# Optimization experiments

Measured on AMD Instinct MI355X. Metric: run time of the kernel, lower is better.

The kernel has to match this reference:

```python
import jax, jax.numpy as jnp
import numpy as np

N = 60000   # nodes
E = 200000  # edges
D = 128     # hidden_dim
H = 4       # heads
C = 128     # out_channels per head (concat=False)
L = 3       # num_layers
VA = 128    # atom vocab
VB = 16     # bond vocab
NEG_SLOPE = 0.2


def setup_inputs():
    key = jax.random.key(0)
    ks = jax.random.split(key, 12)
    f = lambda k, s: (jax.random.normal(k, s, jnp.float32) * 0.05)
    return dict(
        x=jax.random.randint(ks[0], (N,), 0, VA),
        edge_index=jax.random.randint(ks[1], (2, E), 0, N),
        edge_attr=jax.random.randint(ks[2], (E,), 0, VB),
        atom_emb=f(ks[3], (VA, D)),
        bond_emb=f(ks[4], (VB, D)),
        Wl=f(ks[5], (L, D, H * C)), bl=jnp.zeros((L, H * C), jnp.float32),
        Wr=f(ks[6], (L, D, H * C)), br=jnp.zeros((L, H * C), jnp.float32),
        We=f(ks[7], (L, D, H * C)),
        att=f(ks[8], (L, H, C)),
        bias=jnp.zeros((L, C), jnp.float32),
        Wa=f(ks[9], (D, VA)), ba=jnp.zeros((VA,), jnp.float32),
        Wb=f(ks[10], (2 * D, VB)), bb=jnp.zeros((VB,), jnp.float32),
    )


def _gatv2_layer(h, e, src, dst, Wl, bl, Wr, br, We, att, bias):
    # GATv2Conv (PyG), eval mode (dropout off), concat=False -> mean over heads
    xl = (h @ Wl + bl).reshape(N, H, C)   # source transform (lin_l)
    xr = (h @ Wr + br).reshape(N, H, C)   # target transform (lin_r)
    ee = (e @ We).reshape(E, H, C)        # edge projection (lin_edge, no bias)
    m = jax.nn.leaky_relu(xl[src] + xr[dst] + ee, NEG_SLOPE)  # [E,H,C]
    logits = jnp.einsum('ehc,hc->eh', m, att)                 # [E,H]
    # segment-softmax over incoming edges of each target node
    mx = jax.ops.segment_max(logits, dst, num_segments=N)
    a = jnp.exp(logits - mx[dst])
    s = jax.ops.segment_sum(a, dst, num_segments=N)
    alpha = a / (s[dst] + 1e-16)
    agg = jax.ops.segment_sum(alpha[:, :, None] * xl[src], dst, num_segments=N)
    return agg.mean(axis=1) + bias  # [N,D]


def reference(x, edge_index, edge_attr, atom_emb, bond_emb,
              Wl, bl, Wr, br, We, att, bias, Wa, ba, Wb, bb):
    src, dst = edge_index[0], edge_index[1]
    h = atom_emb[x]          # [N,D]
    e = bond_emb[edge_attr]  # [E,D]
    for l in range(L):
        upd = _gatv2_layer(h, e, src, dst, Wl[l], bl[l], Wr[l], br[l],
                           We[l], att[l], bias[l])
        h = h + jax.nn.relu(upd)
    atom_logits = h @ Wa + ba                              # [N,VA]
    pair = jnp.concatenate([h[src], h[dst]], axis=-1)      # [E,2D]
    bond_logits = pair @ Wb + bb                           # [E,VB]
    return atom_logits, bond_logits
```

## Files before the change

kernel.cpp:

```cpp
#include <hip/hip_runtime.h>
#include <hip/hip_bf16.h>
#include <math.h>

#define NN 60000
#define NE 200000
#define DD 128
#define NH 4
#define HC 512
#define NL 3
#define VAv 128
#define VBv 16
#define SCAN_CHUNK 512

typedef __attribute__((ext_vector_type(8))) short bf16x8;
typedef __attribute__((ext_vector_type(4))) float f32x4;

__device__ __forceinline__ float bf2f(unsigned short u){
    union{unsigned int i; float f;} v; v.i = ((unsigned int)u)<<16; return v.f;
}
__device__ __forceinline__ unsigned short f2bf(float f){
    union{float f; unsigned int i;} v; v.f = f;
    unsigned int r = v.i + 0x7fffu + ((v.i>>16)&1u);
    return (unsigned short)(r>>16);
}

#define GLOAD_LDS16(g, l) \
    __builtin_amdgcn_global_load_lds((const __attribute__((address_space(1))) void*)(g), \
                                     (__attribute__((address_space(3))) void*)(l), 16, 0, 0)

__global__ void k_embed(const int* __restrict__ x, const float* __restrict__ atom_emb,
                        float* __restrict__ h, unsigned short* __restrict__ hb) {
    int idx = blockIdx.x*blockDim.x + threadIdx.x;
    if (idx >= NN*(DD/4)) return;
    int n = idx >> 5;
    int c4 = idx & 31;
    int a = x[n];
    float4 v = ((const float4*)(atom_emb + (size_t)a*DD))[c4];
    ((float4*)(h + (size_t)n*DD))[c4] = v;
    ushort4 u = make_ushort4(f2bf(v.x), f2bf(v.y), f2bf(v.z), f2bf(v.w));
    ((ushort4*)(hb + (size_t)n*DD))[c4] = u;
}

__global__ void k_convw(const float* __restrict__ Wl, const float* __restrict__ Wr,
                        const float* __restrict__ bl, const float* __restrict__ br,
                        unsigned short* __restrict__ Wlrt, float* __restrict__ blr) {
    int t = blockIdx.x*256 + threadIdx.x;
    if (t < NL*1024*DD) {
        int l = t / (1024*DD);
        int r = t % (1024*DD);
        int n = r / DD;
        int k = r % DD;
        float v = (n < HC) ? Wl[(size_t)l*DD*HC + (size_t)k*HC + n]
                           : Wr[(size_t)l*DD*HC + (size_t)k*HC + (n - HC)];
        Wlrt[t] = f2bf(v);
    }
    if (t < NL*1024) {
        int l = t / 1024, j = t % 1024;
        blr[t] = (j < HC) ? bl[(size_t)l*HC + j] : br[(size_t)l*HC + (j - HC)];
    }
}

__global__ void k_convwa(const float* __restrict__ Wa, unsigned short* __restrict__ Wat) {
    int t = blockIdx.x*256 + threadIdx.x;
    if (t >= DD*VAv) return;
    int n = t / DD;
    int k = t % DD;
    Wat[t] = f2bf(Wa[(size_t)k*VAv + n]);
}

__global__ void k_eproj(const float* __restrict__ bond_emb, const float* __restrict__ We,
                        float* __restrict__ eprojd) {
    int t = blockIdx.x*256 + threadIdx.x;
    if (t >= NL*VBv*HC) return;
    int n = t & (HC-1);
    int v = (t >> 9) & (VBv-1);
    int l = t >> 13;
    const float* be = bond_emb + (size_t)v*DD;
    const float* w  = We + (size_t)l*DD*HC + n;
    float acc = 0.f;
    #pragma unroll 8
    for (int k = 0; k < DD; ++k) acc = fmaf(be[k], w[(size_t)k*HC], acc);
    int ln = n >> 3, u = n & 7;
    int pos = (u >> 2)*256 + ln*4 + (u & 3);
    eprojd[((size_t)l*VBv + v)*HC + pos] = acc;
}

__global__ void k_deg(const int* __restrict__ dst, int* __restrict__ deg) {
    int e = blockIdx.x*blockDim.x + threadIdx.x;
    if (e < NE) atomicAdd(&deg[dst[e]], 1);
}

__global__ void k_scan1(const int* __restrict__ deg, int* __restrict__ exc, int* __restrict__ sums) {
    __shared__ int buf[2][SCAN_CHUNK];
    int t = threadIdx.x;
    int gi = blockIdx.x*SCAN_CHUNK + t;
    int v = (gi < NN) ? deg[gi] : 0;
    buf[0][t] = v;
    __syncthreads();
    int cur = 0;
    for (int off = 1; off < SCAN_CHUNK; off <<= 1) {
        int nv = buf[cur][t] + ((t >= off) ? buf[cur][t-off] : 0);
        buf[cur^1][t] = nv;
        __syncthreads();
        cur ^= 1;
    }
    if (gi < NN) exc[gi] = buf[cur][t] - v;
    if (t == SCAN_CHUNK-1) sums[blockIdx.x] = buf[cur][t];
}

__global__ void k_scan2(int* sums, int nb) {
    __shared__ int buf[2][128];
    int t = threadIdx.x;
    int v = (t < nb) ? sums[t] : 0;
    buf[0][t] = v;
    __syncthreads();
    int cur = 0;
    for (int off = 1; off < 128; off <<= 1) {
        int nv = buf[cur][t] + ((t >= off) ? buf[cur][t-off] : 0);
        buf[cur^1][t] = nv;
        __syncthreads();
        cur ^= 1;
    }
    if (t < nb) sums[t] = buf[cur][t] - v;
}

__global__ void k_scan3(const int* __restrict__ exc, const int* __restrict__ sums,
                        int* __restrict__ rowptr) {
    int i = blockIdx.x*blockDim.x + threadIdx.x;
    if (i < NN) rowptr[i] = exc[i] + sums[i / SCAN_CHUNK];
    if (i == NN) rowptr[NN] = NE;
}

__global__ void k_scatter(const int* __restrict__ srcv, const int* __restrict__ dst,
                          const int* __restrict__ eattr, const int* __restrict__ rowptr,
                          int* __restrict__ cnt, int* __restrict__ packed) {
    int e = blockIdx.x*blockDim.x + threadIdx.x;
    if (e < NE) {
        int d = dst[e];
        int pos = atomicAdd(&cnt[d], 1);
        packed[rowptr[d] + pos] = srcv[e] | (eattr[e] << 16);
    }
}

template<bool OUT_BF16, int MT>
__global__ __launch_bounds__(256)
void k_gemm_mfma(const unsigned short* __restrict__ A,
                 const unsigned short* __restrict__ Bt,
                 const float* __restrict__ bias, void* __restrict__ Cout,
                 int M, int Nc) {
    __shared__ unsigned short As[2][128*128];
    const int tid = threadIdx.x;
    const int lane = tid & 63;
    const int wave = tid >> 6;
    const int bn = blockIdx.x * 128;
    const int bm0 = blockIdx.y * (128*MT);
    const int l15 = lane & 15;
    const int l4  = lane >> 4;
    const int wm = (wave >> 1) * 64;
    const int wn = (wave & 1) * 64;

    bf16x8 bfr[4][4];
    #pragma unroll
    for (int ks = 0; ks < 4; ++ks)
        #pragma unroll
        for (int ni = 0; ni < 4; ++ni)
            bfr[ks][ni] = *(const bf16x8*)(Bt + (size_t)(bn + wn + ni*16 + l15)*128
                                              + (size_t)(ks*4 + l4)*8);

    float4 bv[4];
    #pragma unroll
    for (int ni = 0; ni < 4; ++ni)
        bv[ni] = bias ? *(const float4*)(bias + bn + wn + ni*16 + l4*4)
                      : make_float4(0.f, 0.f, 0.f, 0.f);

    auto stage = [&](int buf, int bm) {
        #pragma unroll
        for (int it = 0; it < 8; ++it) {
            int slot = it*256 + tid;
            int row  = slot >> 4;
            int cph  = slot & 15;
            int clog = cph ^ (row & 15);
            int arow = bm + row; if (arow >= M) arow = M - 1;
            unsigned short* ldst = &As[buf][(size_t)(it*256 + (tid & ~63))*8];
            GLOAD_LDS16(A + (size_t)arow*128 + clog*8, ldst);
        }
    };

    stage(0, bm0);
    asm volatile("s_waitcnt vmcnt(0)" ::: "memory");
    __syncthreads();

    int cur = 0;
    for (int t = 0; t < MT; ++t) {
        int bm = bm0 + t*128;
        if (bm >= M) break;
        bool pf = (t+1 < MT) && (bm + 128 < M);
        if (pf) stage(cur^1, bm + 128);

        f32x4 acc[4][4];
        #pragma unroll
        for (int i = 0; i < 4; ++i)
            #pragma unroll
            for (int j = 0; j < 4; ++j)
                acc[i][j] = (f32x4){0.f, 0.f, 0.f, 0.f};

        #pragma unroll
        for (int ks = 0; ks < 4; ++ks) {
            bf16x8 af[4];
            int cph = (ks*4 + l4) ^ l15;
            #pragma unroll
            for (int mi = 0; mi < 4; ++mi) {
                int row = wm + mi*16 + l15;
                af[mi] = *(const bf16x8*)(&As[cur][(size_t)row*128 + cph*8]);
            }
            #pragma unroll
            for (int mi = 0; mi < 4; ++mi)
                #pragma unroll
                for (int ni = 0; ni < 4; ++ni)
                    acc[mi][ni] = __builtin_amdgcn_mfma_f32_16x16x32_bf16(bfr[ks][ni], af[mi], acc[mi][ni], 0, 0, 0);
        }

        #pragma unroll
        for (int mi = 0; mi < 4; ++mi) {
            int row = bm + wm + mi*16 + l15;
            bool rok = (row < M);
            #pragma unroll
            for (int ni = 0; ni < 4; ++ni) {
                float v0 = acc[mi][ni][0] + bv[ni].x;
                float v1 = acc[mi][ni][1] + bv[ni].y;
                float v2 = acc[mi][ni][2] + bv[ni].z;
                float v3 = acc[mi][ni][3] + bv[ni].w;
                int colb = bn + wn + ni*16 + l4*4;
                if (rok) {
                    if (OUT_BF16) {
                        unsigned int lo, hi;
                        asm("v_cvt_pk_bf16_f32 %0, %1, %2" : "=v"(lo) : "v"(v0), "v"(v1));
                        asm("v_cvt_pk_bf16_f32 %0, %1, %2" : "=v"(hi) : "v"(v2), "v"(v3));
                        *(uint2*)((unsigned short*)Cout + (size_t)row*Nc + colb) = make_uint2(lo, hi);
                    } else {
                        *(float4*)((float*)Cout + (size_t)row*Nc + colb) = make_float4(v0, v1, v2, v3);
                    }
                }
            }
        }

        if (pf) {
            asm volatile("s_waitcnt vmcnt(16)" ::: "memory");
            __builtin_amdgcn_s_barrier();
        }
        cur ^= 1;
    }
}

__global__ __launch_bounds__(512)
void k_aggregate(const unsigned short* __restrict__ xlr,
                 const float* __restrict__ eprojd,
                 const int* __restrict__ rowptr, const int* __restrict__ packed,
                 const float* __restrict__ att,
                 const float* __restrict__ bias,
                 float* __restrict__ h, unsigned short* __restrict__ hb) {
    __shared__ float eps[VBv*HC];
    {
        const float4* s4 = (const float4*)eprojd;
        float4* d4 = (float4*)eps;
        int t = threadIdx.x;
        #pragma unroll
        for (int i = 0; i < 4; ++i) d4[t + i*512] = s4[t + i*512];
    }
    __syncthreads();

    const int wave = threadIdx.x >> 6;
    const int lane = threadIdx.x & 63;
    const int loff = lane*8;
    const int l4x  = lane*4;

    float attf[8];
    {
        float4 a0 = *(const float4*)(att + loff);
        float4 a1 = *(const float4*)(att + loff + 4);
        attf[0]=a0.x; attf[1]=a0.y; attf[2]=a0.z; attf[3]=a0.w;
        attf[4]=a1.x; attf[5]=a1.y; attf[6]=a1.z; attf[7]=a1.w;
    }

#define EDGE_PROC(vv, eA, eB) do {                                          \
        float xf_[8];                                                       \
        float epv_[8] = {eA.x,eA.y,eA.z,eA.w,eB.x,eB.y,eB.z,eB.w};          \
        float pz_ = 0.f;                                                    \
        _Pragma("unroll")                                                   \
        for (int u = 0; u < 8; ++u) {                                       \
            xf_[u] = bf2f((unsigned short)vv[u]);                           \
            float z_ = xf_[u] + xrf[u] + epv_[u];                           \
            pz_ = fmaf(fmaxf(z_, 0.2f*z_), attf[u], pz_);                   \
        }                                                                   \
        pz_ += __shfl_xor(pz_, 1);                                          \
        pz_ += __shfl_xor(pz_, 2);                                          \
        pz_ += __shfl_xor(pz_, 4);                                          \
        pz_ += __shfl_xor(pz_, 8);                                          \
        float w_ = __expf(pz_);                                             \
        wsum += w_;                                                         \
        _Pragma("unroll")                                                   \
        for (int u = 0; u < 8; ++u) acc[u] = fmaf(w_, xf_[u], acc[u]);      \
    } while (0)

    for (int g = blockIdx.x; g < NN/8; g += gridDim.x) {
        int n = g*8 + wave;

        float xrf[8];
        {
            bf16x8 xv = *(const bf16x8*)(xlr + (size_t)n*1024 + 512 + loff);
            #pragma unroll
            for (int u = 0; u < 8; ++u) xrf[u] = bf2f((unsigned short)xv[u]);
        }

        float acc[8] = {0,0,0,0,0,0,0,0};
        float wsum = 0.f;
        int beg = rowptr[n], end = rowptr[n+1];
        int p = beg;

        for (; p + 4 <= end; p += 4) {
            int pk0 = packed[p],   pk1 = packed[p+1];
            int pk2 = packed[p+2], pk3 = packed[p+3];
            bf16x8 v0 = *(const bf16x8*)(xlr + (size_t)(pk0 & 0xFFFF)*1024 + loff);
            bf16x8 v1 = *(const bf16x8*)(xlr + (size_t)(pk1 & 0xFFFF)*1024 + loff);
            bf16x8 v2 = *(const bf16x8*)(xlr + (size_t)(pk2 & 0xFFFF)*1024 + loff);
            bf16x8 v3 = *(const bf16x8*)(xlr + (size_t)(pk3 & 0xFFFF)*1024 + loff);
            const float* e0 = eps + (pk0 >> 16)*HC;
            const float* e1 = eps + (pk1 >> 16)*HC;
            const float* e2 = eps + (pk2 >> 16)*HC;
            const float* e3 = eps + (pk3 >> 16)*HC;
            float4 eA0 = *(const float4*)(e0 + l4x), eB0 = *(const float4*)(e0 + 256 + l4x);
            float4 eA1 = *(const float4*)(e1 + l4x), eB1 = *(const float4*)(e1 + 256 + l4x);
            float4 eA2 = *(const float4*)(e2 + l4x), eB2 = *(const float4*)(e2 + 256 + l4x);
            float4 eA3 = *(const float4*)(e3 + l4x), eB3 = *(const float4*)(e3 + 256 + l4x);
            EDGE_PROC(v0, eA0, eB0);
            EDGE_PROC(v1, eA1, eB1);
            EDGE_PROC(v2, eA2, eB2);
            EDGE_PROC(v3, eA3, eB3);
        }
        if (p + 2 <= end) {
            int pk0 = packed[p], pk1 = packed[p+1];
            bf16x8 v0 = *(const bf16x8*)(xlr + (size_t)(pk0 & 0xFFFF)*1024 + loff);
            bf16x8 v1 = *(const bf16x8*)(xlr + (size_t)(pk1 & 0xFFFF)*1024 + loff);
            const float* e0 = eps + (pk0 >> 16)*HC;
            const float* e1 = eps + (pk1 >> 16)*HC;
            float4 eA0 = *(const float4*)(e0 + l4x), eB0 = *(const float4*)(e0 + 256 + l4x);
            float4 eA1 = *(const float4*)(e1 + l4x), eB1 = *(const float4*)(e1 + 256 + l4x);
            EDGE_PROC(v0, eA0, eB0);
            EDGE_PROC(v1, eA1, eB1);
            p += 2;
        }
        if (p < end) {
            int pk0 = packed[p];
            bf16x8 v0 = *(const bf16x8*)(xlr + (size_t)(pk0 & 0xFFFF)*1024 + loff);
            const float* e0 = eps + (pk0 >> 16)*HC;
            float4 eA0 = *(const float4*)(e0 + l4x), eB0 = *(const float4*)(e0 + 256 + l4x);
            EDGE_PROC(v0, eA0, eB0);
        }

        float inv = __builtin_amdgcn_rcpf(wsum + 1e-16f);
        float rr[8];
        #pragma unroll
        for (int u = 0; u < 8; ++u) rr[u] = acc[u] * inv;
        #pragma unroll
        for (int u = 0; u < 8; ++u) rr[u] += __shfl_xor(rr[u], 16);
        #pragma unroll
        for (int u = 0; u < 8; ++u) rr[u] += __shfl_xor(rr[u], 32);

        if (lane < 16) {
            int c = lane*8;
            float* hp = h + (size_t)n*DD + c;
            float4 h0 = *(const float4*)hp;
            float4 h1 = *(const float4*)(hp + 4);
            float4 b0 = *(const float4*)(bias + c);
            float4 b1 = *(const float4*)(bias + c + 4);
            float o[8];
            o[0] = h0.x + fmaxf(0.f, fmaf(0.25f, rr[0], b0.x));
            o[1] = h0.y + fmaxf(0.f, fmaf(0.25f, rr[1], b0.y));
            o[2] = h0.z + fmaxf(0.f, fmaf(0.25f, rr[2], b0.z));
            o[3] = h0.w + fmaxf(0.f, fmaf(0.25f, rr[3], b0.w));
            o[4] = h1.x + fmaxf(0.f, fmaf(0.25f, rr[4], b1.x));
            o[5] = h1.y + fmaxf(0.f, fmaf(0.25f, rr[5], b1.y));
            o[6] = h1.z + fmaxf(0.f, fmaf(0.25f, rr[6], b1.z));
            o[7] = h1.w + fmaxf(0.f, fmaf(0.25f, rr[7], b1.w));
            *(float4*)hp       = make_float4(o[0], o[1], o[2], o[3]);
            *(float4*)(hp + 4) = make_float4(o[4], o[5], o[6], o[7]);
            ushort4 u0 = make_ushort4(f2bf(o[0]), f2bf(o[1]), f2bf(o[2]), f2bf(o[3]));
            ushort4 u1 = make_ushort4(f2bf(o[4]), f2bf(o[5]), f2bf(o[6]), f2bf(o[7]));
            unsigned short* hbp = hb + (size_t)n*DD + c;
            *(ushort4*)hbp       = u0;
            *(ushort4*)(hbp + 4) = u1;
        }
    }
#undef EDGE_PROC
}

__global__ __launch_bounds__(256)
void k_bond(const unsigned short* __restrict__ hb,
            const int* __restrict__ srcv, const int* __restrict__ dstv,
            const float* __restrict__ Wb, const float* __restrict__ bb,
            float* __restrict__ out) {
    int e = blockIdx.x*256 + threadIdx.x;
    if (e >= NE) return;
    int s = srcv[e], d = dstv[e];
    const bf16x8* hs = (const bf16x8*)(hb + (size_t)s*DD);
    const bf16x8* hd = (const bf16x8*)(hb + (size_t)d*DD);
    float acc[16];
    #pragma unroll
    for (int j = 0; j < 16; ++j) acc[j] = bb[j];
    for (int c = 0; c < 16; ++c) {
        bf16x8 v = hs[c];
        #pragma unroll
        for (int u = 0; u < 8; ++u) {
            float a = bf2f((unsigned short)v[u]);
            const float* w = Wb + (size_t)(c*8 + u)*16;
            #pragma unroll
            for (int j = 0; j < 16; ++j) acc[j] = fmaf(a, w[j], acc[j]);
        }
    }
    for (int c = 0; c < 16; ++c) {
        bf16x8 v = hd[c];
        #pragma unroll
        for (int u = 0; u < 8; ++u) {
            float a = bf2f((unsigned short)v[u]);
            const float* w = Wb + (size_t)(128 + c*8 + u)*16;
            #pragma unroll
            for (int j = 0; j < 16; ++j) acc[j] = fmaf(a, w[j], acc[j]);
        }
    }
    float4* o = (float4*)(out + (size_t)e*16);
    o[0] = make_float4(acc[0],  acc[1],  acc[2],  acc[3]);
    o[1] = make_float4(acc[4],  acc[5],  acc[6],  acc[7]);
    o[2] = make_float4(acc[8],  acc[9],  acc[10], acc[11]);
    o[3] = make_float4(acc[12], acc[13], acc[14], acc[15]);
}

extern "C" void kernel_launch(void* const* d_in, const int* in_sizes, int n_in,
                              void* d_out, int out_size, void* d_ws, size_t ws_size,
                              hipStream_t stream) {
    const int*   x        = (const int*)d_in[0];
    const int*   edge_idx = (const int*)d_in[1];
    const int*   eattr    = (const int*)d_in[2];
    const float* atom_emb = (const float*)d_in[3];
    const float* bond_emb = (const float*)d_in[4];
    const float* Wl  = (const float*)d_in[5];
    const float* bl  = (const float*)d_in[6];
    const float* Wr  = (const float*)d_in[7];
    const float* br  = (const float*)d_in[8];
    const float* We  = (const float*)d_in[9];
    const float* att = (const float*)d_in[10];
    const float* bias= (const float*)d_in[11];
    const float* Wa  = (const float*)d_in[12];
    const float* ba  = (const float*)d_in[13];
    const float* Wb  = (const float*)d_in[14];
    const float* bb  = (const float*)d_in[15];

    const int* src = edge_idx;
    const int* dst = edge_idx + NE;

    char* p = (char*)d_ws;
    auto alloc = [&](size_t bytes) -> void* {
        void* r = p; p += (bytes + 255) & ~(size_t)255; return r;
    };
    float*          h      = (float*)alloc((size_t)NN*DD*4);
    unsigned short* hb     = (unsigned short*)alloc((size_t)NN*DD*2);
    unsigned short* xlr    = (unsigned short*)alloc((size_t)NN*1024*2);
    unsigned short* Wlrt   = (unsigned short*)alloc((size_t)NL*1024*DD*2);
    float*          blr    = (float*)alloc((size_t)NL*1024*4);
    unsigned short* Wat    = (unsigned short*)alloc((size_t)DD*VAv*2);
    float*          eprojd = (float*)alloc((size_t)NL*VBv*HC*4);
    int*            deg    = (int*)alloc((size_t)NN*4);
    int*            exc    = (int*)alloc((size_t)NN*4);
    int*            sums   = (int*)alloc(256*4);
    int*            rowptr = (int*)alloc((size_t)(NN+1)*4);
    int*            cnt    = (int*)alloc((size_t)NN*4);
    int*            packed = (int*)alloc((size_t)NE*4);

    float* atom_out = (float*)d_out;
    float* bond_out = atom_out + (size_t)NN*VAv;

    hipMemsetAsync(deg, 0, (size_t)NN*4, stream);
    hipMemsetAsync(cnt, 0, (size_t)NN*4, stream);

    k_embed<<<7500, 256, 0, stream>>>(x, atom_emb, h, hb);
    k_convw<<<(NL*1024*DD + 255)/256, 256, 0, stream>>>(Wl, Wr, bl, br, Wlrt, blr);
    k_convwa<<<(DD*VAv + 255)/256, 256, 0, stream>>>(Wa, Wat);
    k_eproj<<<(NL*VBv*HC + 255)/256, 256, 0, stream>>>(bond_emb, We, eprojd);

    int nchunks = (NN + SCAN_CHUNK - 1) / SCAN_CHUNK;
    k_deg<<<(NE+255)/256, 256, 0, stream>>>(dst, deg);
    k_scan1<<<nchunks, SCAN_CHUNK, 0, stream>>>(deg, exc, sums);
    k_scan2<<<1, 128, 0, stream>>>(sums, nchunks);
    k_scan3<<<(NN+256)/256, 256, 0, stream>>>(exc, sums, rowptr);
    k_scatter<<<(NE+255)/256, 256, 0, stream>>>(src, dst, eattr, rowptr, cnt, packed);

    const int MTILES = (NN + 127) / 128;
    const int GRP4 = (MTILES + 3) / 4;
    const int GRP2 = (MTILES + 1) / 2;
    for (int l = 0; l < NL; ++l) {
        const float* att_l  = att  + (size_t)l*NH*VAv;
        const float* bias_l = bias + (size_t)l*DD;
        const unsigned short* Wlrt_l = Wlrt + (size_t)l*1024*DD;
        const float* blr_l = blr + (size_t)l*1024;
        const float* ep_l  = eprojd + (size_t)l*VBv*HC;

        k_gemm_mfma<true, 4><<<dim3(1024/128, GRP4), 256, 0, stream>>>(hb, Wlrt_l, blr_l, xlr, NN, 1024);
        k_aggregate<<<2500, 512, 0, stream>>>(xlr, ep_l, rowptr, packed, att_l, bias_l, h, hb);
    }

    k_gemm_mfma<false, 2><<<dim3(VAv/128, GRP2), 256, 0, stream>>>(hb, Wat, ba, atom_out, NN, VAv);
    k_bond<<<(NE+255)/256, 256, 0, stream>>>(hb, src, dst, Wb, bb, bond_out);
}
```

Measured before the change: 472.7 us.

## Use MFMA for bond logits and swizzle GEMM block order for L2 reuse

```diff
diff --git a/kernel.cpp b/kernel.cpp
--- a/kernel.cpp
+++ b/kernel.cpp
@@ -66,6 +66,13 @@
     int n = t / DD;
     int k = t % DD;
     Wat[t] = f2bf(Wa[(size_t)k*VAv + n]);
+}
+
+__global__ void k_convwb(const float* __restrict__ Wb, unsigned short* __restrict__ Wbt) {
+    int t = blockIdx.x*256 + threadIdx.x;
+    if (t >= 16*256) return;
+    int c = t >> 8, k = t & 255;
+    Wbt[t] = f2bf(Wb[(size_t)k*16 + c]);
 }
 
 __global__ void k_eproj(const float* __restrict__ bond_emb, const float* __restrict__ We,
@@ -142,18 +149,29 @@
     }
 }
 
-template<bool OUT_BF16, int MT>
+template<bool OUT_BF16, int MT, bool SWZ>
 __global__ __launch_bounds__(256)
 void k_gemm_mfma(const unsigned short* __restrict__ A,
                  const unsigned short* __restrict__ Bt,
                  const float* __restrict__ bias, void* __restrict__ Cout,
-                 int M, int Nc) {
+                 int M, int Nc, int NP) {
     __shared__ unsigned short As[2][128*128];
     const int tid = threadIdx.x;
     const int lane = tid & 63;
     const int wave = tid >> 6;
-    const int bn = blockIdx.x * 128;
-    const int bm0 = blockIdx.y * (128*MT);
+
+    int bn, bm0;
+    if (SWZ) {
+        int F = blockIdx.x;
+        int P = (F & 7) + ((F >> 6) << 3);
+        if (P >= NP) return;
+        bn  = ((F >> 3) & 7) * 128;
+        bm0 = P * (128*MT);
+    } else {
+        bn  = blockIdx.x * 128;
+        bm0 = blockIdx.y * (128*MT);
+    }
+
     const int l15 = lane & 15;
     const int l4  = lane >> 4;
     const int wm = (wave >> 1) * 64;
@@ -397,41 +415,36 @@
 __global__ __launch_bounds__(256)
 void k_bond(const unsigned short* __restrict__ hb,
             const int* __restrict__ srcv, const int* __restrict__ dstv,
-            const float* __restrict__ Wb, const float* __restrict__ bb,
+            const unsigned short* __restrict__ Wbt, const float* __restrict__ bb,
             float* __restrict__ out) {
-    int e = blockIdx.x*256 + threadIdx.x;
-    if (e >= NE) return;
-    int s = srcv[e], d = dstv[e];
-    const bf16x8* hs = (const bf16x8*)(hb + (size_t)s*DD);
-    const bf16x8* hd = (const bf16x8*)(hb + (size_t)d*DD);
-    float acc[16];
+    int lane = threadIdx.x & 63;
+    int wave = threadIdx.x >> 6;
+    int ebase = blockIdx.x*64 + wave*16;
+    int l15 = lane & 15, l4 = lane >> 4;
+    int e = ebase + l15;
+    const unsigned short* hs = hb + (size_t)srcv[e]*DD;
+    const unsigned short* hd = hb + (size_t)dstv[e]*DD;
+
+    bf16x8 bfr[8];
     #pragma unroll
-    for (int j = 0; j < 16; ++j) acc[j] = bb[j];
-    for (int c = 0; c < 16; ++c) {
-        bf16x8 v = hs[c];
-        #pragma unroll
-        for (int u = 0; u < 8; ++u) {
-            float a = bf2f((unsigned short)v[u]);
-            const float* w = Wb + (size_t)(c*8 + u)*16;
-            #pragma unroll
-            for (int j = 0; j < 16; ++j) acc[j] = fmaf(a, w[j], acc[j]);
-        }
-    }
-    for (int c = 0; c < 16; ++c) {
-        bf16x8 v = hd[c];
-        #pragma unroll
-        for (int u = 0; u < 8; ++u) {
-            float a = bf2f((unsigned short)v[u]);
-            const float* w = Wb + (size_t)(128 + c*8 + u)*16;
-            #pragma unroll
-            for (int j = 0; j < 16; ++j) acc[j] = fmaf(a, w[j], acc[j]);
-        }
-    }
-    float4* o = (float4*)(out + (size_t)e*16);
-    o[0] = make_float4(acc[0],  acc[1],  acc[2],  acc[3]);
-    o[1] = make_float4(acc[4],  acc[5],  acc[6],  acc[7]);
-    o[2] = make_float4(acc[8],  acc[9],  acc[10], acc[11]);
-    o[3] = make_float4(acc[12], acc[13], acc[14], acc[15]);
+    for (int s = 0; s < 8; ++s)
+        bfr[s] = *(const bf16x8*)(Wbt + l15*256 + s*32 + l4*8);
+
+    float bbv = bb[l15];
+    f32x4 acc = (f32x4){bbv, bbv, bbv, bbv};
+    #pragma unroll
+    for (int s = 0; s < 4; ++s) {
+        bf16x8 af = *(const bf16x8*)(hs + s*32 + l4*8);
+        acc = __builtin_amdgcn_mfma_f32_16x16x32_bf16(af, bfr[s], acc, 0, 0, 0);
+    }
+    #pragma unroll
+    for (int s = 0; s < 4; ++s) {
+        bf16x8 af = *(const bf16x8*)(hd + s*32 + l4*8);
+        acc = __builtin_amdgcn_mfma_f32_16x16x32_bf16(af, bfr[4+s], acc, 0, 0, 0);
+    }
+    #pragma unroll
+    for (int r = 0; r < 4; ++r)
+        out[(size_t)(ebase + l4*4 + r)*16 + l15] = acc[r];
 }
 
 extern "C" void kernel_launch(void* const* d_in, const int* in_sizes, int n_in,
@@ -467,6 +480,7 @@
     unsigned short* Wlrt   = (unsigned short*)alloc((size_t)NL*1024*DD*2);
     float*          blr    = (float*)alloc((size_t)NL*1024*4);
     unsigned short* Wat    = (unsigned short*)alloc((size_t)DD*VAv*2);
+    unsigned short* Wbt    = (unsigned short*)alloc((size_t)16*256*2);
     float*          eprojd = (float*)alloc((size_t)NL*VBv*HC*4);
     int*            deg    = (int*)alloc((size_t)NN*4);
     int*            exc    = (int*)alloc((size_t)NN*4);
@@ -484,6 +498,7 @@
     k_embed<<<7500, 256, 0, stream>>>(x, atom_emb, h, hb);
     k_convw<<<(NL*1024*DD + 255)/256, 256, 0, stream>>>(Wl, Wr, bl, br, Wlrt, blr);
     k_convwa<<<(DD*VAv + 255)/256, 256, 0, stream>>>(Wa, Wat);
+    k_convwb<<<16, 256, 0, stream>>>(Wb, Wbt);
     k_eproj<<<(NL*VBv*HC + 255)/256, 256, 0, stream>>>(bond_emb, We, eprojd);
 
     int nchunks = (NN + SCAN_CHUNK - 1) / SCAN_CHUNK;
@@ -496,6 +511,7 @@
     const int MTILES = (NN + 127) / 128;
     const int GRP4 = (MTILES + 3) / 4;
     const int GRP2 = (MTILES + 1) / 2;
+    const int SWZ_BLKS = ((GRP4 + 7) / 8) * 64;
     for (int l = 0; l < NL; ++l) {
         const float* att_l  = att  + (size_t)l*NH*VAv;
         const float* bias_l = bias + (size_t)l*DD;
@@ -503,10 +519,10 @@
         const float* blr_l = blr + (size_t)l*1024;
         const float* ep_l  = eprojd + (size_t)l*VBv*HC;
 
-        k_gemm_mfma<true, 4><<<dim3(1024/128, GRP4), 256, 0, stream>>>(hb, Wlrt_l, blr_l, xlr, NN, 1024);
+        k_gemm_mfma<true, 4, true><<<SWZ_BLKS, 256, 0, stream>>>(hb, Wlrt_l, blr_l, xlr, NN, 1024, GRP4);
         k_aggregate<<<2500, 512, 0, stream>>>(xlr, ep_l, rowptr, packed, att_l, bias_l, h, hb);
     }
 
-    k_gemm_mfma<false, 2><<<dim3(VAv/128, GRP2), 256, 0, stream>>>(hb, Wat, ba, atom_out, NN, VAv);
-    k_bond<<<(NE+255)/256, 256, 0, stream>>>(hb, src, dst, Wb, bb, bond_out);
-}
+    k_gemm_mfma<false, 2, false><<<dim3(VAv/128, GRP2), 256, 0, stream>>>(hb, Wat, ba, atom_out, NN, VAv, GRP2);
+    k_bond<<<NE/64, 256, 0, stream>>>(hb, src, dst, Wbt, bb, bond_out);
+}
```

Result: faster. 447.9 us (-5.2%).
